# Kernel optimization log

Measured on AMD Instinct MI355X. Metric: run time of the kernel, lower is better.

## Reference

```python
import jax, jax.numpy as jnp
import numpy as np

# Dropout layers are treated as identity (eval mode); note the original Adaptive
# module references self.dropout without defining it, so train mode would error anyway.

def setup_inputs() -> dict:
    key = jax.random.key(0)
    ks = jax.random.split(key, 13)
    B, T, H, E2, VOC, K = 128, 64, 512, 1024, 10000, 49
    s = lambda *sh: 1.0 / np.sqrt(sh[-1])
    return {
        "x":       jax.random.normal(ks[0], (B, T, E2), jnp.float32),
        "hiddens": jax.random.normal(ks[1], (B, T, H), jnp.float32),
        "cells":   jax.random.normal(ks[2], (B, T, H), jnp.float32),
        "V":       jax.random.normal(ks[3], (B, K, H), jnp.float32),
        # attention params
        "Wv": jax.random.normal(ks[4], (K, H), jnp.float32) * s(K, H),
        "Wg": jax.random.normal(ks[5], (K, H), jnp.float32) * s(K, H),
        "Ws": jax.random.normal(ks[6], (K, H), jnp.float32) * s(K, H),
        "wh": jax.random.normal(ks[7], (K,), jnp.float32) * s(K,),
        # sentinel params
        "Wx":  jax.random.normal(ks[8], (H, E2), jnp.float32) * s(H, E2),
        "Wsh": jax.random.normal(ks[9], (H, H), jnp.float32) * s(H, H),
        # output mlp
        "Wm": jax.random.normal(ks[10], (VOC, H), jnp.float32) * s(VOC, H),
        "bm": jnp.zeros((VOC,), jnp.float32),
    }


def reference(x, hiddens, cells, V, Wv, Wg, Ws, wh, Wx, Wsh, Wm, bm):
    B, T, H = hiddens.shape
    # h_{t-1}: zero init state prepended, last hidden dropped
    h0 = jnp.zeros((B, 1, H), hiddens.dtype)
    hiddens_t_1 = jnp.concatenate([h0, hiddens[:, :-1, :]], axis=1) if T > 1 else h0

    # Sentinel gate: sent_t = sigmoid(x Wx^T + h_{t-1} Wh^T) * tanh(cells)
    gate = jnp.einsum('bte,he->bth', x, Wx) + jnp.einsum('btj,hj->bth', hiddens_t_1, Wsh)
    sent = jax.nn.sigmoid(gate) * jnp.tanh(cells)            # [B,T,H]

    # Additive attention over K=49 spatial features
    cv = jnp.einsum('bkh,nh->bkn', V, Wv)                    # [B,K,49]
    cg = jnp.einsum('bth,nh->btn', hiddens, Wg)              # [B,T,49]
    content = jnp.tanh(cv[:, None, :, :] + cg[:, :, None, :])  # [B,T,K,49]
    z = jnp.einsum('btkn,n->btk', content, wh)               # [B,T,K]
    alpha = jax.nn.softmax(z, axis=-1)                       # [B,T,K]
    c = jnp.einsum('btk,bkh->bth', alpha, V)                 # [B,T,H]

    # Sentinel-extended softmax -> beta
    cs = jnp.einsum('bth,nh->btn', sent, Ws) + cg            # [B,T,49]
    z_ext = jnp.einsum('btn,n->bt', jnp.tanh(cs), wh)[..., None]  # [B,T,1]
    extend = jnp.concatenate([z, z_ext], axis=-1)            # [B,T,K+1]
    alpha_hat = jax.nn.softmax(extend, axis=-1)
    beta = alpha_hat[:, :, -1:]                              # [B,T,1]

    c_hat = beta * sent + (1.0 - beta) * c                   # [B,T,H]
    output = jnp.einsum('bth,vh->btv', c_hat + hiddens, Wm) + bm  # [B,T,vocab]
    return output, alpha, beta
```

## Files before the change

kernel.cpp:

```cpp
#include <hip/hip_runtime.h>
#include <hip/hip_bf16.h>
#include <math.h>

typedef __bf16 bf16;
typedef __bf16 bf16x4 __attribute__((ext_vector_type(4)));
typedef __bf16 bf16x8 __attribute__((ext_vector_type(8)));
typedef float f32x4 __attribute__((ext_vector_type(4)));

#define BB  128
#define TT  64
#define BTT 8192
#define HH  512
#define EE  1024
#define KA  49
#define NV  10000

__device__ __forceinline__ float ftanh(float x) {
    float cx = fminf(fmaxf(x, -15.f), 15.f);
    float e = __expf(2.f * cx);
    return (e - 1.f) * __builtin_amdgcn_rcpf(e + 1.f);
}
__device__ __forceinline__ float fsigmoid(float x) {
    return __builtin_amdgcn_rcpf(1.f + __expf(-x));
}

__device__ __forceinline__ void cvt4(const float* __restrict__ s, bf16* __restrict__ d) {
    f32x4 v = *(const f32x4*)s;
    bf16x4 o = { (bf16)v[0], (bf16)v[1], (bf16)v[2], (bf16)v[3] };
    *(bf16x4*)d = o;
}
__device__ __forceinline__ void cvt4nt(const float* __restrict__ s, bf16* __restrict__ d) {
    f32x4 v = __builtin_nontemporal_load((const f32x4*)s);
    bf16x4 o = { (bf16)v[0], (bf16)v[1], (bf16)v[2], (bf16)v[3] };
    *(bf16x4*)d = o;
}

__global__ __launch_bounds__(256)
void prep_kernel(const float* __restrict__ x, const float* __restrict__ hid,
                 const float* __restrict__ V, const float* __restrict__ Wv,
                 const float* __restrict__ Wg, const float* __restrict__ Ws,
                 const float* __restrict__ Wx, const float* __restrict__ Wsh,
                 bf16* __restrict__ xb, bf16* __restrict__ hb,
                 bf16* __restrict__ Vb, bf16* __restrict__ Wvb, bf16* __restrict__ Wgb,
                 bf16* __restrict__ Wsb, bf16* __restrict__ Wxb, bf16* __restrict__ Wshb,
                 bf16* __restrict__ zbuf)
{
    if (blockIdx.x == 0 && threadIdx.x < 128) {
        bf16x8 z = {};
        *(bf16x8*)(zbuf + threadIdx.x * 8) = z;
    }

    const long NX = (long)BTT * EE;
    const long NH = (long)BTT * HH;
    const long NVV = (long)BB * KA * HH;
    const long NWX = (long)HH * EE;
    const long NWSH = (long)HH * HH;
    const long NW = (long)KA * HH;
    const long total4 = (NX + NH + NVV + NWX + NWSH + 3 * NW) >> 2;

    long t0 = (long)blockIdx.x * 256 + threadIdx.x;
    long st = (long)gridDim.x * 256;
    for (long i4 = t0; i4 < total4; i4 += st) {
        long i = i4 << 2;
        if (i < NX) { cvt4nt(x + i, xb + i); continue; }
        i -= NX;
        if (i < NH) { cvt4(hid + i, hb + i); continue; }
        i -= NH;
        if (i < NVV) { cvt4nt(V + i, Vb + i); continue; }
        i -= NVV;
        if (i < NWX) { cvt4nt(Wx + i, Wxb + i); continue; }
        i -= NWX;
        if (i < NWSH) { cvt4nt(Wsh + i, Wshb + i); continue; }
        i -= NWSH;
        if (i < NW) { cvt4nt(Wv + i, Wvb + i); continue; }
        i -= NW;
        if (i < NW) { cvt4nt(Wg + i, Wgb + i); continue; }
        i -= NW;
        cvt4nt(Ws + i, Wsb + i);
    }
}

template<int EPI, bool SHIFT>
__device__ __forceinline__ void gemm128_core(
    bf16* smem,
    const bf16* __restrict__ A1, const bf16* __restrict__ B1, int K1,
    const bf16* __restrict__ A2, const bf16* __restrict__ B2, int K2,
    int N, const float* __restrict__ eaux, void* __restrict__ outv, int ldo,
    int bm0, int bn0, const bf16* __restrict__ zbuf)
{
    const int tid = threadIdx.x;
    const int lane = tid & 63;
    const int wid = tid >> 6;
    const int wm = (wid >> 1) * 64;
    const int wn = (wid & 1) * 64;
    const int rA = lane & 15;
    const int ks = lane >> 4;
    const int swzB = (ks ^ ((rA >> 1) & 3)) * 16;

    const int c0 = tid, c1 = tid + 256;
    const int row0 = c0 >> 2, row1 = c1 >> 2;
    const int gc0 = ((c0 & 3) ^ ((row0 >> 1) & 3)) * 8;
    const int gc1 = ((c1 & 3) ^ ((row1 >> 1) & 3)) * 8;
    const int br0 = (bn0 + row0 < N) ? bn0 + row0 : N - 1;
    const int br1 = (bn0 + row1 < N) ? bn0 + row1 : N - 1;

    const int NT1 = K1 >> 5;
    const int NT2 = K2 >> 5;
    const int NT = NT1 + NT2;

    const bf16* A1r0 = A1 + (size_t)(bm0 + row0) * K1 + gc0;
    const bf16* A1r1 = A1 + (size_t)(bm0 + row1) * K1 + gc1;
    const bf16* B1r0 = B1 + (size_t)br0 * K1 + gc0;
    const bf16* B1r1 = B1 + (size_t)br1 * K1 + gc1;
    const bf16 *A2r0 = nullptr, *A2r1 = nullptr, *B2r0 = nullptr, *B2r1 = nullptr;
    if (K2 > 0) {
        if (SHIFT) {
            A2r0 = (((bm0 + row0) & 63) == 0) ? zbuf + gc0
                                              : A2 + (size_t)(bm0 + row0 - 1) * K2 + gc0;
            A2r1 = (((bm0 + row1) & 63) == 0) ? zbuf + gc1
                                              : A2 + (size_t)(bm0 + row1 - 1) * K2 + gc1;
        } else {
            A2r0 = A2 + (size_t)(bm0 + row0) * K2 + gc0;
            A2r1 = A2 + (size_t)(bm0 + row1) * K2 + gc1;
        }
        B2r0 = B2 + (size_t)br0 * K2 + gc0;
        B2r1 = B2 + (size_t)br1 * K2 + gc1;
    }

    auto stage = [&](int t) {
        const bf16 *a0, *a1, *b0, *b1; int k0;
        if (t < NT1) { k0 = t << 5;          a0 = A1r0; a1 = A1r1; b0 = B1r0; b1 = B1r1; }
        else         { k0 = (t - NT1) << 5;  a0 = A2r0; a1 = A2r1; b0 = B2r0; b1 = B2r1; }
        char* base = (char*)smem + (t & 3) * 16384;
        __builtin_amdgcn_global_load_lds(
            (const __attribute__((address_space(1))) unsigned int*)(a0 + k0),
            (__attribute__((address_space(3))) unsigned int*)(base + c0 * 16), 16, 0, 0);
        __builtin_amdgcn_global_load_lds(
            (const __attribute__((address_space(1))) unsigned int*)(a1 + k0),
            (__attribute__((address_space(3))) unsigned int*)(base + c1 * 16), 16, 0, 0);
        __builtin_amdgcn_global_load_lds(
            (const __attribute__((address_space(1))) unsigned int*)(b0 + k0),
            (__attribute__((address_space(3))) unsigned int*)(base + 8192 + c0 * 16), 16, 0, 0);
        __builtin_amdgcn_global_load_lds(
            (const __attribute__((address_space(1))) unsigned int*)(b1 + k0),
            (__attribute__((address_space(3))) unsigned int*)(base + 8192 + c1 * 16), 16, 0, 0);
    };

    f32x4 acc[4][4] = {};

    stage(0); stage(1); stage(2);
    asm volatile("s_waitcnt vmcnt(8)" ::: "memory");
    __builtin_amdgcn_s_barrier();

    for (int t = 0; t < NT; ++t) {
        const char* sA = (const char*)smem + (t & 3) * 16384;
        const char* sB = sA + 8192;

        bf16x8 af[4], bfr[4];
        #pragma unroll
        for (int mi = 0; mi < 4; ++mi)
            af[mi] = *(const bf16x8*)(sA + (wm + mi * 16 + rA) * 64 + swzB);
        #pragma unroll
        for (int ni = 0; ni < 4; ++ni)
            bfr[ni] = *(const bf16x8*)(sB + (wn + ni * 16 + rA) * 64 + swzB);

        if (t + 3 < NT) {
            stage(t + 3);
            asm volatile("s_waitcnt vmcnt(8)" ::: "memory");
        } else if (t + 2 < NT) {
            asm volatile("s_waitcnt vmcnt(4)" ::: "memory");
        } else {
            asm volatile("s_waitcnt vmcnt(0)" ::: "memory");
        }
        __builtin_amdgcn_s_barrier();

        __builtin_amdgcn_s_setprio(1);
        #pragma unroll
        for (int mi = 0; mi < 4; ++mi) {
            #pragma unroll
            for (int ni = 0; ni < 4; ++ni)
                acc[mi][ni] = __builtin_amdgcn_mfma_f32_16x16x32_bf16(af[mi], bfr[ni], acc[mi][ni], 0, 0, 0);
        }
        __builtin_amdgcn_s_setprio(0);
        __builtin_amdgcn_s_barrier();
    }

    #pragma unroll
    for (int mi = 0; mi < 4; ++mi) {
        #pragma unroll
        for (int ni = 0; ni < 4; ++ni) {
            const int col = bn0 + wn + ni * 16 + rA;
            if (col < N) {
                #pragma unroll
                for (int r = 0; r < 4; ++r) {
                    const int rowg = bm0 + wm + mi * 16 + ks * 4 + r;
                    float v = acc[mi][ni][r];
                    if (EPI == 0) {
                        ((bf16*)outv)[(size_t)rowg * ldo + col] =
                            (bf16)(fsigmoid(v) * ftanh(eaux[(size_t)rowg * ldo + col]));
                    } else {
                        ((float*)outv)[(size_t)rowg * ldo + col] = v;
                    }
                }
            }
        }
    }
}

__global__ __launch_bounds__(256, 2)
void gate_mid128(const bf16* __restrict__ xb, const bf16* __restrict__ Wxb,
                 const bf16* __restrict__ Wshb,
                 const float* __restrict__ cel, bf16* __restrict__ sentb,
                 const bf16* __restrict__ Vb, const bf16* __restrict__ Wvb,
                 const bf16* __restrict__ hb, const bf16* __restrict__ Wgb,
                 float* __restrict__ cv, float* __restrict__ cg,
                 const float* __restrict__ Wm, bf16* __restrict__ Wmb,
                 const bf16* __restrict__ zbuf)
{
    __shared__ bf16 smem[4 * 8192];
    const int bid = blockIdx.x;
    if (bid >= 369) {
        const long n4 = ((long)NV * HH) >> 2;
        for (long i4 = (long)(bid - 369) * 256 + threadIdx.x; i4 < n4; i4 += 143L * 256)
            cvt4nt(Wm + (i4 << 2), Wmb + (i4 << 2));
        return;
    }
    if (bid < 256) {
        const int bm0 = (bid >> 2) * 128;
        const int bn0 = (bid & 3) * 128;
        gemm128_core<0, true>(smem, xb, Wxb, EE, hb, Wshb, HH, HH, cel, (void*)sentb, HH,
                              bm0, bn0, zbuf);
    } else if (bid < 305) {
        gemm128_core<2, false>(smem, Vb, Wvb, HH, nullptr, nullptr, 0, KA, nullptr,
                               (void*)cv, KA, (bid - 256) * 128, 0, nullptr);
    } else {
        gemm128_core<2, false>(smem, hb, Wgb, HH, nullptr, nullptr, 0, KA, nullptr,
                               (void*)cg, KA, (bid - 305) * 128, 0, nullptr);
    }
}

__global__ __launch_bounds__(256, 2)
void cs64(const bf16* __restrict__ sentb, const bf16* __restrict__ Wsb,
          float* __restrict__ cs)
{
    __shared__ bf16 smem[4 * 4096];
    const int bm0 = blockIdx.x * 64;
    const int tid = threadIdx.x;
    const int lane = tid & 63;
    const int w = tid >> 6;
    const int rA = lane & 15;
    const int ks = lane >> 4;
    const int swzB = (ks ^ ((rA >> 1) & 3)) * 16;

    const int row = tid >> 2;
    const int gc = ((tid & 3) ^ ((row >> 1) & 3)) * 8;
    const int browc = (row < KA) ? row : KA - 1;
    const bf16* Ar = sentb + (size_t)(bm0 + row) * HH + gc;
    const bf16* Br = Wsb + (size_t)browc * HH + gc;

    auto stage = [&](int t) {
        char* base = (char*)smem + (t & 3) * 8192;
        const int k0 = t << 5;
        __builtin_amdgcn_global_load_lds(
            (const __attribute__((address_space(1))) unsigned int*)(Ar + k0),
            (__attribute__((address_space(3))) unsigned int*)(base + tid * 16), 16, 0, 0);
        __builtin_amdgcn_global_load_lds(
            (const __attribute__((address_space(1))) unsigned int*)(Br + k0),
            (__attribute__((address_space(3))) unsigned int*)(base + 4096 + tid * 16), 16, 0, 0);
    };

    f32x4 acc[4] = {};
    const int NT = HH / 32;

    stage(0); stage(1); stage(2);
    asm volatile("s_waitcnt vmcnt(4)" ::: "memory");
    __builtin_amdgcn_s_barrier();

    for (int t = 0; t < NT; ++t) {
        const char* sA = (const char*)smem + (t & 3) * 8192;
        const char* sB = sA + 4096;

        bf16x8 af[4];
        #pragma unroll
        for (int mi = 0; mi < 4; ++mi)
            af[mi] = *(const bf16x8*)(sA + (mi * 16 + rA) * 64 + swzB);
        bf16x8 bfr = *(const bf16x8*)(sB + (w * 16 + rA) * 64 + swzB);

        if (t + 3 < NT) {
            stage(t + 3);
            asm volatile("s_waitcnt vmcnt(4)" ::: "memory");
        } else if (t + 2 < NT) {
            asm volatile("s_waitcnt vmcnt(2)" ::: "memory");
        } else {
            asm volatile("s_waitcnt vmcnt(0)" ::: "memory");
        }
        __builtin_amdgcn_s_barrier();

        __builtin_amdgcn_s_setprio(1);
        #pragma unroll
        for (int mi = 0; mi < 4; ++mi)
            acc[mi] = __builtin_amdgcn_mfma_f32_16x16x32_bf16(af[mi], bfr, acc[mi], 0, 0, 0);
        __builtin_amdgcn_s_setprio(0);
        __builtin_amdgcn_s_barrier();
    }

    const int col = w * 16 + rA;
    if (col < KA) {
        #pragma unroll
        for (int mi = 0; mi < 4; ++mi) {
            #pragma unroll
            for (int r = 0; r < 4; ++r) {
                const int rowg = bm0 + mi * 16 + ks * 4 + r;
                cs[(size_t)rowg * KA + col] = acc[mi][r];
            }
        }
    }
}

__global__ __launch_bounds__(256)
void softz_kernel(const float* __restrict__ cv, const float* __restrict__ cg,
                  const float* __restrict__ cs, const float* __restrict__ wh,
                  float* __restrict__ alpha, float* __restrict__ beta)
{
    __shared__ float cvL[KA * KA];
    __shared__ float whL[64];
    __shared__ float cgL[4 * KA];

    const int tid = threadIdx.x;
    const int w = tid >> 6, lane = tid & 63;
    const int bt0 = blockIdx.x * 4;
    const int b = bt0 >> 6;
    const int bt = bt0 + w;

    const float* cvb = cv + (size_t)b * KA * KA;
    for (int i = tid; i < KA * KA; i += 256) cvL[i] = cvb[i];
    if (tid < KA) whL[tid] = wh[tid];
    if (lane < KA) cgL[w * KA + lane] = cg[(size_t)bt * KA + lane];
    float csv0 = (lane < KA) ? cs[(size_t)bt * KA + lane] : 0.f;
    __syncthreads();

    float z = -INFINITY;
    if (lane < KA) {
        const float* cvk = cvL + lane * KA;
        const float* cgr = cgL + w * KA;
        float acc = 0.f;
        #pragma unroll 7
        for (int n = 0; n < KA; ++n)
            acc += ftanh(cvk[n] + cgr[n]) * whL[n];
        z = acc;
    }
    const float csv = csv0 + ((lane < KA) ? cgL[w * KA + lane] : 0.f);
    float u = (lane < KA) ? ftanh(csv) * whL[lane] : 0.f;

    float m1 = z;
    #pragma unroll
    for (int o = 32; o; o >>= 1) m1 = fmaxf(m1, __shfl_xor(m1, o, 64));
    float e = (lane < KA) ? __expf(z - m1) : 0.f;
    float s1 = e, ze = u;
    #pragma unroll
    for (int o = 32; o; o >>= 1) { s1 += __shfl_xor(s1, o, 64); ze += __shfl_xor(ze, o, 64); }

    if (lane < KA) alpha[(size_t)bt * KA + lane] = e / s1;
    if (lane == 0) {
        float M2 = fmaxf(m1, ze);
        float denom = s1 * __expf(m1 - M2) + __expf(ze - M2);
        beta[bt] = __expf(ze - M2) / denom;
    }
}

__global__ __launch_bounds__(256)
void cch_kernel(const float* __restrict__ alpha, const float* __restrict__ beta,
                const bf16* __restrict__ Vb, const bf16* __restrict__ sentb,
                const float* __restrict__ hid, bf16* __restrict__ chb)
{
    __shared__ float aL[TT * KA];
    __shared__ float bL[TT];

    const int b = blockIdx.x >> 3;
    const int hc = blockIdx.x & 7;
    const int tid = threadIdx.x;
    const int w = tid >> 6, lane = tid & 63;
    const int h = hc * 64 + lane;

    const float* ab = alpha + (size_t)b * TT * KA;
    for (int i = tid; i < TT * KA; i += 256) aL[i] = ab[i];
    if (tid < TT) bL[tid] = beta[b * TT + tid];

    float vreg[KA];
    #pragma unroll
    for (int k = 0; k < KA; ++k) vreg[k] = (float)Vb[((size_t)b * KA + k) * HH + h];
    __syncthreads();

    #pragma unroll 1
    for (int tt = 0; tt < 16; ++tt) {
        const int t = w * 16 + tt;
        const int bt = b * TT + t;
        const float* ar = aL + t * KA;
        float c = 0.f;
        #pragma unroll
        for (int k = 0; k < KA; ++k) c += ar[k] * vreg[k];
        const float be = bL[t];
        const size_t idx = (size_t)bt * HH + h;
        float ch = be * (float)sentb[idx] + (1.f - be) * c
                 + __builtin_nontemporal_load(hid + idx);
        chb[idx] = (bf16)ch;
    }
}

__global__ __launch_bounds__(512, 4)
void gemm256x128_bias(const bf16* __restrict__ A, const bf16* __restrict__ B,
                      const float* __restrict__ bias, float* __restrict__ out)
{
    const int K = HH;
    const int N = NV;
    const int NT = K / 32;
    const int ntn = 79;

    __shared__ bf16 smem[3 * 12288];

    const int bid = blockIdx.x;
    const int wg = (bid & 7) * 316 + (bid >> 3);
    const int bm0 = (wg / ntn) * 256;
    const int bn0 = (wg % ntn) * 128;

    const int tid = threadIdx.x;
    const int lane = tid & 63;
    const int wid = tid >> 6;
    const int wr = (wid >> 1) * 64;
    const int wc = (wid & 1) * 64;
    const int rA = lane & 15;
    const int ks = lane >> 4;
    const int swz = (ks ^ ((rA >> 1) & 3)) * 16;

    const int arow0 = tid >> 2;
    const int arow1 = arow0 + 128;
    const int gcA0 = ((tid & 3) ^ ((arow0 >> 1) & 3)) * 8;
    const int gcA1 = ((tid & 3) ^ ((arow1 >> 1) & 3)) * 8;
    const int brow = tid >> 2;
    const int gcB  = ((tid & 3) ^ ((brow >> 1) & 3)) * 8;
    const int browc = (bn0 + brow < N) ? bn0 + brow : N - 1;

    const bf16* Ap0 = A + (size_t)(bm0 + arow0) * K + gcA0;
    const bf16* Ap1 = A + (size_t)(bm0 + arow1) * K + gcA1;
    const bf16* Bp  = B + (size_t)browc * K + gcB;

    auto stage = [&](int t, int slot) {
        char* base = (char*)smem + slot * 24576;
        const int k0 = t << 5;
        __builtin_amdgcn_global_load_lds(
            (const __attribute__((address_space(1))) unsigned int*)(Ap0 + k0),
            (__attribute__((address_space(3))) unsigned int*)(base + tid * 16), 16, 0, 0);
        __builtin_amdgcn_global_load_lds(
            (const __attribute__((address_space(1))) unsigned int*)(Ap1 + k0),
            (__attribute__((address_space(3))) unsigned int*)(base + (tid + 512) * 16), 16, 0, 0);
        __builtin_amdgcn_global_load_lds(
            (const __attribute__((address_space(1))) unsigned int*)(Bp + k0),
            (__attribute__((address_space(3))) unsigned int*)(base + 16384 + tid * 16), 16, 0, 0);
    };

    f32x4 acc[4][4] = {};

    stage(0, 0); stage(1, 1);
    asm volatile("s_waitcnt vmcnt(3)" ::: "memory");
    __builtin_amdgcn_s_barrier();

    int slR = 0, slS = 2;
    for (int t = 0; t < NT; ++t) {
        const char* sA = (const char*)smem + slR * 24576;
        const char* sB = sA + 16384;

        bf16x8 af[4], bfr[4];
        #pragma unroll
        for (int mi = 0; mi < 4; ++mi)
            af[mi] = *(const bf16x8*)(sA + (wr + mi * 16 + rA) * 64 + swz);
        #pragma unroll
        for (int ni = 0; ni < 4; ++ni)
            bfr[ni] = *(const bf16x8*)(sB + (wc + ni * 16 + rA) * 64 + swz);

        if (t + 2 < NT) {
            stage(t + 2, slS);
            asm volatile("s_waitcnt vmcnt(3)" ::: "memory");
        } else {
            asm volatile("s_waitcnt vmcnt(0)" ::: "memory");
        }
        __builtin_amdgcn_s_barrier();

        __builtin_amdgcn_s_setprio(1);
        #pragma unroll
        for (int mi = 0; mi < 4; ++mi) {
            #pragma unroll
            for (int ni = 0; ni < 4; ++ni)
                acc[mi][ni] = __builtin_amdgcn_mfma_f32_16x16x32_bf16(af[mi], bfr[ni], acc[mi][ni], 0, 0, 0);
        }
        __builtin_amdgcn_s_setprio(0);
        __builtin_amdgcn_s_barrier();

        slR = (slR == 2) ? 0 : slR + 1;
        slS = (slS == 2) ? 0 : slS + 1;
    }

    float bv[4];
    #pragma unroll
    for (int ni = 0; ni < 4; ++ni) {
        const int col = bn0 + wc + ni * 16 + rA;
        bv[ni] = (col < N) ? bias[col] : 0.f;
    }
    float* lt = (float*)smem + wid * 2048;
    #pragma unroll
    for (int half = 0; half < 2; ++half) {
        #pragma unroll
        for (int mi2 = 0; mi2 < 2; ++mi2) {
            const int mi = half * 2 + mi2;
            #pragma unroll
            for (int ni = 0; ni < 4; ++ni) {
                #pragma unroll
                for (int r = 0; r < 4; ++r) {
                    const int row = mi2 * 16 + ks * 4 + r;
                    const int col = ni * 16 + rA;
                    const int s = ((((row >> 2) & 3) ^ (row & 3)) << 4);
                    lt[row * 64 + (col ^ s)] = acc[mi][ni][r] + bv[ni];
                }
            }
        }
        #pragma unroll
        for (int i = 0; i < 8; ++i) {
            const int row = i * 4 + ks;
            const int c0 = rA * 4;
            const int s = ((((row >> 2) & 3) ^ (row & 3)) << 4);
            f32x4 v = *(const f32x4*)&lt[row * 64 + (c0 ^ s)];
            const int rowg = bm0 + wr + half * 32 + row;
            const int colg = bn0 + wc + c0;
            if (colg < N)
                __builtin_nontemporal_store(v, (f32x4*)&out[(size_t)rowg * N + colg]);
        }
    }
}

extern "C" void kernel_launch(void* const* d_in, const int* in_sizes, int n_in,
                              void* d_out, int out_size, void* d_ws, size_t ws_size,
                              hipStream_t stream)
{
    const float* x   = (const float*)d_in[0];
    const float* hid = (const float*)d_in[1];
    const float* cel = (const float*)d_in[2];
    const float* V   = (const float*)d_in[3];
    const float* Wv  = (const float*)d_in[4];
    const float* Wg  = (const float*)d_in[5];
    const float* Ws  = (const float*)d_in[6];
    const float* wh  = (const float*)d_in[7];
    const float* Wx  = (const float*)d_in[8];
    const float* Wsh = (const float*)d_in[9];
    const float* Wm  = (const float*)d_in[10];
    const float* bm  = (const float*)d_in[11];

    float* out_o   = (float*)d_out;
    float* alpha_o = out_o + (size_t)BTT * NV;
    float* beta_o  = alpha_o + (size_t)BTT * KA;

    char* p = (char*)d_ws;
    bf16* sentb = (bf16*)p; p += (size_t)BTT * HH * 2;
    bf16* chb   = (bf16*)p; p += (size_t)BTT * HH * 2;
    bf16* xb    = (bf16*)p; p += (size_t)BTT * EE * 2;
    bf16* hb    = (bf16*)p; p += (size_t)BTT * HH * 2;
    bf16* Vb    = (bf16*)p; p += (size_t)BB * KA * HH * 2;
    bf16* Wxb   = (bf16*)p; p += (size_t)HH * EE * 2;
    bf16* Wshb  = (bf16*)p; p += (size_t)HH * HH * 2;
    bf16* Wmb   = (bf16*)p; p += (size_t)NV * HH * 2;
    bf16* Wvb   = (bf16*)p; p += (size_t)KA * HH * 2;
    bf16* Wgb   = (bf16*)p; p += (size_t)KA * HH * 2;
    bf16* Wsb   = (bf16*)p; p += (size_t)KA * HH * 2;
    bf16* zbuf  = (bf16*)p; p += 1024 * 2;
    float* cv   = (float*)p; p += (size_t)BB * KA * KA * 4;
    float* cg   = (float*)p; p += (size_t)BTT * KA * 4;
    float* cs   = (float*)p; p += (size_t)BTT * KA * 4;

    prep_kernel<<<2048, 256, 0, stream>>>(x, hid, V, Wv, Wg, Ws, Wx, Wsh,
                                          xb, hb, Vb, Wvb, Wgb, Wsb, Wxb, Wshb, zbuf);

    gate_mid128<<<512, 256, 0, stream>>>(xb, Wxb, Wshb, cel, sentb,
                                         Vb, Wvb, hb, Wgb, cv, cg, Wm, Wmb, zbuf);

    cs64<<<128, 256, 0, stream>>>(sentb, Wsb, cs);

    softz_kernel<<<BTT / 4, 256, 0, stream>>>(cv, cg, cs, wh, alpha_o, beta_o);
    cch_kernel<<<BB * 8, 256, 0, stream>>>(alpha_o, beta_o, Vb, sentb, hid, chb);

    gemm256x128_bias<<<32 * 79, 512, 0, stream>>>(chb, Wmb, bm, out_o);
}
```

Before: 217.6 us.

## Fuse x fp32-to-bf16 conversion into gate GEMM via direct fp32 LDS staging

Stops converting x (8192x1024 fp32) to bf16 in the prep kernel. The gate GEMM instead loads fp32 x tiles straight into LDS with global_load_lds and converts them to bf16 when reading fragments. It also uses a 3-slot async pipeline and a swizzled block-to-tile mapping. This removes one full write and read of a 16MB intermediate. In exchange the GEMM moves twice the bytes for x, needs more LDS (72KB, which may limit occupancy), and adds conversion work to its inner loop.

```diff
diff --git a/kernel.cpp b/kernel.cpp
--- a/kernel.cpp
+++ b/kernel.cpp
@@ -36,11 +36,11 @@
 }
 
 __global__ __launch_bounds__(256)
-void prep_kernel(const float* __restrict__ x, const float* __restrict__ hid,
+void prep_kernel(const float* __restrict__ hid,
                  const float* __restrict__ V, const float* __restrict__ Wv,
                  const float* __restrict__ Wg, const float* __restrict__ Ws,
                  const float* __restrict__ Wx, const float* __restrict__ Wsh,
-                 bf16* __restrict__ xb, bf16* __restrict__ hb,
+                 bf16* __restrict__ hb,
                  bf16* __restrict__ Vb, bf16* __restrict__ Wvb, bf16* __restrict__ Wgb,
                  bf16* __restrict__ Wsb, bf16* __restrict__ Wxb, bf16* __restrict__ Wshb,
                  bf16* __restrict__ zbuf)
@@ -50,20 +50,17 @@
         *(bf16x8*)(zbuf + threadIdx.x * 8) = z;
     }
 
-    const long NX = (long)BTT * EE;
     const long NH = (long)BTT * HH;
     const long NVV = (long)BB * KA * HH;
     const long NWX = (long)HH * EE;
     const long NWSH = (long)HH * HH;
     const long NW = (long)KA * HH;
-    const long total4 = (NX + NH + NVV + NWX + NWSH + 3 * NW) >> 2;
+    const long total4 = (NH + NVV + NWX + NWSH + 3 * NW) >> 2;
 
     long t0 = (long)blockIdx.x * 256 + threadIdx.x;
     long st = (long)gridDim.x * 256;
     for (long i4 = t0; i4 < total4; i4 += st) {
         long i = i4 << 2;
-        if (i < NX) { cvt4nt(x + i, xb + i); continue; }
-        i -= NX;
         if (i < NH) { cvt4(hid + i, hb + i); continue; }
         i -= NH;
         if (i < NVV) { cvt4nt(V + i, Vb + i); continue; }
@@ -207,8 +204,149 @@
     }
 }
 
+__device__ __forceinline__ void gate128f(
+    char* smem, const float* __restrict__ xf, const bf16* __restrict__ Wxb,
+    const bf16* __restrict__ hb, const bf16* __restrict__ Wshb,
+    const float* __restrict__ cel, bf16* __restrict__ sentb,
+    int bm0, int bn0, const bf16* __restrict__ zbuf)
+{
+    const int NT1 = EE >> 5;
+    const int NT = NT1 + (HH >> 5);
+
+    const int tid = threadIdx.x;
+    const int lane = tid & 63;
+    const int wid = tid >> 6;
+    const int wm = (wid >> 1) * 64;
+    const int wn = (wid & 1) * 64;
+    const int rA = lane & 15;
+    const int ks = lane >> 4;
+    const int swzB = (ks ^ ((rA >> 1) & 3)) * 16;
+
+    const float* xsrc[4];
+    #pragma unroll
+    for (int j = 0; j < 4; ++j) {
+        const int c = tid + 256 * j;
+        const int row = c >> 3, slot = c & 7;
+        xsrc[j] = xf + (size_t)(bm0 + row) * EE + ((slot ^ ((row >> 1) & 7)) << 2);
+    }
+    const int cb0 = tid, cb1 = tid + 256;
+    const int brow0 = cb0 >> 2, brow1 = cb1 >> 2;
+    const int gb0 = ((cb0 & 3) ^ ((brow0 >> 1) & 3)) * 8;
+    const int gb1 = ((cb1 & 3) ^ ((brow1 >> 1) & 3)) * 8;
+
+    const bf16* B1r0 = Wxb + (size_t)(bn0 + brow0) * EE + gb0;
+    const bf16* B1r1 = Wxb + (size_t)(bn0 + brow1) * EE + gb1;
+    const bf16* B2r0 = Wshb + (size_t)(bn0 + brow0) * HH + gb0;
+    const bf16* B2r1 = Wshb + (size_t)(bn0 + brow1) * HH + gb1;
+    const bf16* A2r0 = (((bm0 + brow0) & 63) == 0) ? zbuf + gb0
+                                                   : hb + (size_t)(bm0 + brow0 - 1) * HH + gb0;
+    const bf16* A2r1 = (((bm0 + brow1) & 63) == 0) ? zbuf + gb1
+                                                   : hb + (size_t)(bm0 + brow1 - 1) * HH + gb1;
+
+    auto stage = [&](int t, int slot) {
+        char* base = smem + slot * 24576;
+        if (t < NT1) {
+            const int k0 = t << 5;
+            #pragma unroll
+            for (int j = 0; j < 4; ++j)
+                __builtin_amdgcn_global_load_lds(
+                    (const __attribute__((address_space(1))) unsigned int*)(xsrc[j] + k0),
+                    (__attribute__((address_space(3))) unsigned int*)(base + (tid + 256 * j) * 16), 16, 0, 0);
+            __builtin_amdgcn_global_load_lds(
+                (const __attribute__((address_space(1))) unsigned int*)(B1r0 + k0),
+                (__attribute__((address_space(3))) unsigned int*)(base + 16384 + cb0 * 16), 16, 0, 0);
+            __builtin_amdgcn_global_load_lds(
+                (const __attribute__((address_space(1))) unsigned int*)(B1r1 + k0),
+                (__attribute__((address_space(3))) unsigned int*)(base + 16384 + cb1 * 16), 16, 0, 0);
+        } else {
+            const int k0 = (t - NT1) << 5;
+            __builtin_amdgcn_global_load_lds(
+                (const __attribute__((address_space(1))) unsigned int*)(A2r0 + k0),
+                (__attribute__((address_space(3))) unsigned int*)(base + cb0 * 16), 16, 0, 0);
+            __builtin_amdgcn_global_load_lds(
+                (const __attribute__((address_space(1))) unsigned int*)(A2r1 + k0),
+                (__attribute__((address_space(3))) unsigned int*)(base + cb1 * 16), 16, 0, 0);
+            __builtin_amdgcn_global_load_lds(
+                (const __attribute__((address_space(1))) unsigned int*)(B2r0 + k0),
+                (__attribute__((address_space(3))) unsigned int*)(base + 16384 + cb0 * 16), 16, 0, 0);
+            __builtin_amdgcn_global_load_lds(
+                (const __attribute__((address_space(1))) unsigned int*)(B2r1 + k0),
+                (__attribute__((address_space(3))) unsigned int*)(base + 16384 + cb1 * 16), 16, 0, 0);
+        }
+    };
+
+    f32x4 acc[4][4] = {};
+
+    stage(0, 0); stage(1, 1);
+    asm volatile("s_waitcnt vmcnt(6)" ::: "memory");
+    __builtin_amdgcn_s_barrier();
+
+    int slR = 0, slS = 2;
+    for (int t = 0; t < NT; ++t) {
+        const char* base = smem + slR * 24576;
+        const char* sB = base + 16384;
+
+        bf16x8 af[4], bfr[4];
+        if (t < NT1) {
+            #pragma unroll
+            for (int mi = 0; mi < 4; ++mi) {
+                const int row = wm + mi * 16 + rA;
+                const int m = (row >> 1) & 7;
+                f32x4 lo = *(const f32x4*)(base + row * 128 + (((2 * ks) ^ m) << 4));
+                f32x4 hi = *(const f32x4*)(base + row * 128 + (((2 * ks + 1) ^ m) << 4));
+                bf16x8 v = { (bf16)lo[0], (bf16)lo[1], (bf16)lo[2], (bf16)lo[3],
+                             (bf16)hi[0], (bf16)hi[1], (bf16)hi[2], (bf16)hi[3] };
+                af[mi] = v;
+            }
+        } else {
+            #pragma unroll
+            for (int mi = 0; mi < 4; ++mi)
+                af[mi] = *(const bf16x8*)(base + (wm + mi * 16 + rA) * 64 + swzB);
+        }
+        #pragma unroll
+        for (int ni = 0; ni < 4; ++ni)
+            bfr[ni] = *(const bf16x8*)(sB + (wn + ni * 16 + rA) * 64 + swzB);
+
+        if (t + 2 < NT) {
+            stage(t + 2, slS);
+            if (t + 2 < NT1) asm volatile("s_waitcnt vmcnt(6)" ::: "memory");
+            else             asm volatile("s_waitcnt vmcnt(4)" ::: "memory");
+        } else {
+            asm volatile("s_waitcnt vmcnt(0)" ::: "memory");
+        }
+        __builtin_amdgcn_s_barrier();
+
+        __builtin_amdgcn_s_setprio(1);
+        #pragma unroll
+        for (int mi = 0; mi < 4; ++mi) {
+            #pragma unroll
+            for (int ni = 0; ni < 4; ++ni)
+                acc[mi][ni] = __builtin_amdgcn_mfma_f32_16x16x32_bf16(af[mi], bfr[ni], acc[mi][ni], 0, 0, 0);
+        }
+        __builtin_amdgcn_s_setprio(0);
+        __builtin_amdgcn_s_barrier();
+
+        slR = (slR == 2) ? 0 : slR + 1;
+        slS = (slS == 2) ? 0 : slS + 1;
+    }
+
+    #pragma unroll
+    for (int mi = 0; mi < 4; ++mi) {
+        #pragma unroll
+        for (int ni = 0; ni < 4; ++ni) {
+            const int col = bn0 + wn + ni * 16 + rA;
+            #pragma unroll
+            for (int r = 0; r < 4; ++r) {
+                const int rowg = bm0 + wm + mi * 16 + ks * 4 + r;
+                sentb[(size_t)rowg * HH + col] =
+                    (bf16)(fsigmoid(acc[mi][ni][r]) * ftanh(cel[(size_t)rowg * HH + col]));
+            }
+        }
+    }
+}
+
 __global__ __launch_bounds__(256, 2)
-void gate_mid128(const bf16* __restrict__ xb, const bf16* __restrict__ Wxb,
+void gate_mid128(const float* __restrict__ xf, const bf16* __restrict__ Wxb,
                  const bf16* __restrict__ Wshb,
                  const float* __restrict__ cel, bf16* __restrict__ sentb,
                  const bf16* __restrict__ Vb, const bf16* __restrict__ Wvb,
@@ -217,7 +355,7 @@
                  const float* __restrict__ Wm, bf16* __restrict__ Wmb,
                  const bf16* __restrict__ zbuf)
 {
-    __shared__ bf16 smem[4 * 8192];
+    __shared__ char smem[73728];
     const int bid = blockIdx.x;
     if (bid >= 369) {
         const long n4 = ((long)NV * HH) >> 2;
@@ -226,15 +364,14 @@
         return;
     }
     if (bid < 256) {
-        const int bm0 = (bid >> 2) * 128;
-        const int bn0 = (bid & 3) * 128;
-        gemm128_core<0, true>(smem, xb, Wxb, EE, hb, Wshb, HH, HH, cel, (void*)sentb, HH,
-                              bm0, bn0, zbuf);
+        const int lin = (bid & 7) * 32 + (bid >> 3);
+        gate128f(smem, xf, Wxb, hb, Wshb, cel, sentb,
+                 (lin >> 2) * 128, (lin & 3) * 128, zbuf);
     } else if (bid < 305) {
-        gemm128_core<2, false>(smem, Vb, Wvb, HH, nullptr, nullptr, 0, KA, nullptr,
+        gemm128_core<2, false>((bf16*)smem, Vb, Wvb, HH, nullptr, nullptr, 0, KA, nullptr,
                                (void*)cv, KA, (bid - 256) * 128, 0, nullptr);
     } else {
-        gemm128_core<2, false>(smem, hb, Wgb, HH, nullptr, nullptr, 0, KA, nullptr,
+        gemm128_core<2, false>((bf16*)smem, hb, Wgb, HH, nullptr, nullptr, 0, KA, nullptr,
                                (void*)cg, KA, (bid - 305) * 128, 0, nullptr);
     }
 }
@@ -560,7 +697,6 @@
     char* p = (char*)d_ws;
     bf16* sentb = (bf16*)p; p += (size_t)BTT * HH * 2;
     bf16* chb   = (bf16*)p; p += (size_t)BTT * HH * 2;
-    bf16* xb    = (bf16*)p; p += (size_t)BTT * EE * 2;
     bf16* hb    = (bf16*)p; p += (size_t)BTT * HH * 2;
     bf16* Vb    = (bf16*)p; p += (size_t)BB * KA * HH * 2;
     bf16* Wxb   = (bf16*)p; p += (size_t)HH * EE * 2;
@@ -574,10 +710,10 @@
     float* cg   = (float*)p; p += (size_t)BTT * KA * 4;
     float* cs   = (float*)p; p += (size_t)BTT * KA * 4;
 
-    prep_kernel<<<2048, 256, 0, stream>>>(x, hid, V, Wv, Wg, Ws, Wx, Wsh,
-                                          xb, hb, Vb, Wvb, Wgb, Wsb, Wxb, Wshb, zbuf);
-
-    gate_mid128<<<512, 256, 0, stream>>>(xb, Wxb, Wshb, cel, sentb,
+    prep_kernel<<<2048, 256, 0, stream>>>(hid, V, Wv, Wg, Ws, Wx, Wsh,
+                                          hb, Vb, Wvb, Wgb, Wsb, Wxb, Wshb, zbuf);
+
+    gate_mid128<<<512, 256, 0, stream>>>(x, Wxb, Wshb, cel, sentb,
                                          Vb, Wvb, hb, Wgb, cv, cg, Wm, Wmb, zbuf);
 
     cs64<<<128, 256, 0, stream>>>(sentb, Wsb, cs);
```

New measurement: 206.0 us. -5.3%, faster.
